# Kernel optimization log

Measured on AMD Instinct MI355X. Metric: run time of the kernel, lower is better.

## Reference

```python
import jax, jax.numpy as jnp
import numpy as np

N = 50000
D = 128
E = 600000
R = 8


def setup_inputs() -> dict:
    key = jax.random.key(0)
    ks = jax.random.split(key, 8)
    x = jax.random.normal(ks[0], (N, D), dtype=jnp.float32)
    edge_index = jax.random.randint(ks[1], (2, E), 0, N, dtype=jnp.int64)
    edge_type = jax.random.randint(ks[2], (E,), 0, R, dtype=jnp.int64)
    scale = 1.0 / np.sqrt(D)
    w1 = jax.random.normal(ks[3], (R, D, D), dtype=jnp.float32) * scale
    root1 = jax.random.normal(ks[4], (D, D), dtype=jnp.float32) * scale
    b1 = jnp.zeros((D,), dtype=jnp.float32)
    w2 = jax.random.normal(ks[5], (R, D, D), dtype=jnp.float32) * scale
    root2 = jax.random.normal(ks[6], (D, D), dtype=jnp.float32) * scale
    b2 = jnp.zeros((D,), dtype=jnp.float32)
    return {"x": x, "edge_index": edge_index, "edge_type": edge_type,
            "w1": w1, "root1": root1, "b1": b1,
            "w2": w2, "root2": root2, "b2": b2}


def _rgcn_conv(x, edge_index, edge_type, w, root, b):
    # PyG RGCNConv: per-relation MEAN aggregation of source features over
    # incoming edges, then relation-specific linear, summed over relations,
    # plus root transform and bias.
    src, dst = edge_index[0], edge_index[1]
    # combined segment id: (dst_node, relation) -> one segment_sum pass
    seg = dst * R + edge_type  # [E]
    msgs = x[src]              # [E, D] gather
    sums = jax.ops.segment_sum(msgs, seg, num_segments=N * R).reshape(N, R, D)
    cnts = jax.ops.segment_sum(jnp.ones((msgs.shape[0],), dtype=x.dtype), seg,
                               num_segments=N * R).reshape(N, R, 1)
    mean = sums / jnp.maximum(cnts, 1.0)  # [N, R, D]; empty -> 0
    out = jnp.einsum('nrd,rde->ne', mean, w) + x @ root + b
    return out


def reference(x, edge_index, edge_type, w1, root1, b1, w2, root2, b2):
    # dropout is identity in eval mode
    h = jax.nn.relu(_rgcn_conv(x, edge_index, edge_type, w1, root1, b1))
    out = jax.nn.relu(_rgcn_conv(h, edge_index, edge_type, w2, root2, b2))
    return out
```

## Files before the change

kernel.cpp:

```cpp
#include <hip/hip_runtime.h>

#define NN 50000
#define D 128
#define EE 600000
#define R 8
#define NR (NN * R)
#define SCAN_CHUNK 1024
#define NSB ((NR + SCAN_CHUNK - 1) / SCAN_CHUNK)
#define KO 1152

typedef unsigned short u16;
typedef unsigned int u32;
typedef __attribute__((ext_vector_type(8))) short bf16x8;
typedef __attribute__((ext_vector_type(4))) float f32x4;

__device__ inline u16 f2bf(float f) {
    union { float f; u32 u; } v; v.f = f;
    return (u16)((v.u + 0x7FFFu + ((v.u >> 16) & 1u)) >> 16);
}
__device__ inline float bf2f(u16 h) {
    union { u32 u; float f; } v; v.u = ((u32)h) << 16;
    return v.f;
}

__global__ __launch_bounds__(256) void xcast_kernel(const float2* __restrict__ x2,
                                                    u32* __restrict__ xb, int n) {
    int i = blockIdx.x * 256 + threadIdx.x;
    if (i < n) {
        float2 v = x2[i];
        xb[i] = (u32)f2bf(v.x) | ((u32)f2bf(v.y) << 16);
    }
}

__global__ __launch_bounds__(256) void hist_kernel(const int* __restrict__ dst,
                                                   const int* __restrict__ et,
                                                   int* __restrict__ cnt, int E) {
    int e = blockIdx.x * 256 + threadIdx.x;
    if (e < E) atomicAdd(&cnt[dst[e] * R + et[e]], 1);
}

__global__ __launch_bounds__(256) void scanA(const int* __restrict__ cnt,
                                             int* __restrict__ off,
                                             int* __restrict__ bsum) {
    __shared__ int ts[256];
    const int b = blockIdx.x, t = threadIdx.x;
    const int base = b * SCAN_CHUNK + t * 4;
    int v0 = 0, v1 = 0, v2 = 0, v3 = 0;
    if (base + 3 < NR) {
        int4 q = *(const int4*)(cnt + base);
        v0 = q.x; v1 = q.y; v2 = q.z; v3 = q.w;
    } else {
        if (base < NR) v0 = cnt[base];
        if (base + 1 < NR) v1 = cnt[base + 1];
        if (base + 2 < NR) v2 = cnt[base + 2];
    }
    const int s = v0 + v1 + v2 + v3;
    ts[t] = s;
    __syncthreads();
    for (int d = 1; d < 256; d <<= 1) {
        int x = (t >= d) ? ts[t - d] : 0;
        __syncthreads();
        ts[t] += x;
        __syncthreads();
    }
    const int excl = ts[t] - s;
    if (base < NR) off[base] = excl;
    if (base + 1 < NR) off[base + 1] = excl + v0;
    if (base + 2 < NR) off[base + 2] = excl + v0 + v1;
    if (base + 3 < NR) off[base + 3] = excl + v0 + v1 + v2;
    if (t == 255) bsum[b] = ts[255];
}

__global__ __launch_bounds__(512) void scanB(const int* __restrict__ bsum,
                                             int* __restrict__ boff) {
    __shared__ int ts[512];
    const int t = threadIdx.x;
    const int v = (t < NSB) ? bsum[t] : 0;
    ts[t] = v;
    __syncthreads();
    for (int d = 1; d < 512; d <<= 1) {
        int x = (t >= d) ? ts[t - d] : 0;
        __syncthreads();
        ts[t] += x;
        __syncthreads();
    }
    if (t < NSB) boff[t] = ts[t] - v;
}

__global__ __launch_bounds__(256) void scanC(int* __restrict__ off,
                                             int* __restrict__ cursor,
                                             const int* __restrict__ boff) {
    const int b = blockIdx.x, t = threadIdx.x;
    const int add = boff[b];
    const int base = b * SCAN_CHUNK + t * 4;
#pragma unroll
    for (int j = 0; j < 4; ++j)
        if (base + j < NR) {
            int v = off[base + j] + add;
            off[base + j] = v;
            cursor[base + j] = v;
        }
    if (b == 0 && t == 0) off[NR] = EE;
}

__global__ __launch_bounds__(256) void place_kernel(const int* __restrict__ src,
                                                    const int* __restrict__ dst,
                                                    const int* __restrict__ et,
                                                    const int* __restrict__ cnt,
                                                    int* __restrict__ cursor,
                                                    u32* __restrict__ epos,
                                                    float* __restrict__ scale, int E) {
    int e = blockIdx.x * 256 + threadIdx.x;
    if (e < E) {
        int r = et[e];
        int key = dst[e] * R + r;
        int p = atomicAdd(&cursor[key], 1);
        epos[p] = (u32)src[e] * (KO / 2) + (u32)r * (D / 2);
        scale[p] = 1.0f / (float)cnt[key];
    }
}

__global__ __launch_bounds__(256) void bprep2_kernel(const float* __restrict__ w1,
                                                     const float* __restrict__ root1,
                                                     u16* __restrict__ Bf1,
                                                     const float* __restrict__ w2,
                                                     const float* __restrict__ root2,
                                                     u16* __restrict__ Bf2) {
    int gidx = blockIdx.x * 256 + threadIdx.x;
    if (gidx >= 2 * 9 * 4 * 8 * 64) return;
    const int layer = gidx / (9 * 4 * 8 * 64);
    const int idx = gidx - layer * (9 * 4 * 8 * 64);
    const float* w = layer ? w2 : w1;
    const float* root = layer ? root2 : root1;
    u16* Bfrag = layer ? Bf2 : Bf1;
    const int lane = idx & 63;
    const int g = (idx >> 6) & 7;
    const int kc = (idx >> 9) & 3;
    const int ct = idx >> 11;
    const int col = ct * 128 + g * 16 + (lane & 15);
    const int kbase = kc * 32 + (lane >> 4) * 8;
    u16* o = Bfrag + (size_t)idx * 8;
#pragma unroll
    for (int j = 0; j < 8; ++j) {
        const int k = kbase + j;
        float v = (col < R * D) ? w[(size_t)(col >> 7) * (D * D) + (size_t)k * D + (col & 127)]
                                : root[(size_t)k * D + (col - R * D)];
        o[j] = f2bf(v);
    }
}

__global__ __launch_bounds__(256) void gemm_xw(const u16* __restrict__ xin,
                                               const u16* __restrict__ Bfrag,
                                               u16* __restrict__ y) {
    __shared__ uint4 Bs[2048];

    const int t = threadIdx.x;
    const int wave = t >> 6;
    const int lane = t & 63;
    const int quad = lane >> 4;
    const int l15 = lane & 15;
    const int n0 = blockIdx.x * 64;
    const int ct = blockIdx.y;
    const int n = n0 + wave * 16 + l15;
    const int nc = (n < NN) ? n : (NN - 1);

    const uint4* bsrc = (const uint4*)Bfrag + (size_t)ct * 2048;
    uint4 s[8];
#pragma unroll
    for (int i = 0; i < 8; ++i) s[i] = bsrc[t + 256 * i];

    const u16* xr = xin + (size_t)nc * D + quad * 8;
    bf16x8 a0 = *(const bf16x8*)(xr);
    bf16x8 a1 = *(const bf16x8*)(xr + 32);
    bf16x8 a2 = *(const bf16x8*)(xr + 64);
    bf16x8 a3 = *(const bf16x8*)(xr + 96);

#pragma unroll
    for (int i = 0; i < 8; ++i) Bs[t + 256 * i] = s[i];
    __syncthreads();

    f32x4 acc[8];
#pragma unroll
    for (int g = 0; g < 8; ++g) acc[g] = (f32x4){0.f, 0.f, 0.f, 0.f};

    const u16* bb = (const u16*)Bs + lane * 8;
#pragma unroll
    for (int g = 0; g < 8; ++g) {
        bf16x8 b0 = *(const bf16x8*)(bb + (0 * 8 + g) * 512);
        acc[g] = __builtin_amdgcn_mfma_f32_16x16x32_bf16(a0, b0, acc[g], 0, 0, 0);
        bf16x8 b1 = *(const bf16x8*)(bb + (1 * 8 + g) * 512);
        acc[g] = __builtin_amdgcn_mfma_f32_16x16x32_bf16(a1, b1, acc[g], 0, 0, 0);
        bf16x8 b2 = *(const bf16x8*)(bb + (2 * 8 + g) * 512);
        acc[g] = __builtin_amdgcn_mfma_f32_16x16x32_bf16(a2, b2, acc[g], 0, 0, 0);
        bf16x8 b3 = *(const bf16x8*)(bb + (3 * 8 + g) * 512);
        acc[g] = __builtin_amdgcn_mfma_f32_16x16x32_bf16(a3, b3, acc[g], 0, 0, 0);
    }

#pragma unroll
    for (int g = 0; g < 8; ++g) {
        const int col = ct * 128 + g * 16 + l15;
#pragma unroll
        for (int q = 0; q < 4; ++q) {
            const int row = n0 + wave * 16 + quad * 4 + q;
            if (row < NN)
                y[(size_t)row * KO + col] = f2bf(acc[g][q]);
        }
    }
}

template <bool OUTBF>
__global__ __launch_bounds__(256) void agg_kernel(const u32* __restrict__ yv,
                                                  const int* __restrict__ off,
                                                  const u32* __restrict__ epos,
                                                  const float* __restrict__ scale,
                                                  const float* __restrict__ bias,
                                                  void* __restrict__ outp) {
    const int n = blockIdx.x * 4 + (threadIdx.x >> 6);
    const int lane = threadIdx.x & 63;
    const int e0 = off[n * 8], e1 = off[n * 8 + 8];

    float ax = 0.f, ay = 0.f;
    int cbase = e0;
    u32 ed = 0; float sc = 0.f;
    if (cbase + lane < e1) { ed = epos[cbase + lane]; sc = scale[cbase + lane]; }

    int i = e0;
    while (i < e1) {
        const int chunk_end = (e1 < cbase + 64) ? e1 : (cbase + 64);
        for (; i + 1 < chunk_end; i += 2) {
            const int j0 = i - cbase;
            const u32 p0 = (u32)__shfl((int)ed, j0);
            const u32 p1 = (u32)__shfl((int)ed, j0 + 1);
            const float f0 = __shfl(sc, j0);
            const float f1 = __shfl(sc, j0 + 1);
            const u32 v0 = yv[(size_t)p0 + lane];
            const u32 v1 = yv[(size_t)p1 + lane];
            ax += f0 * bf2f((u16)(v0 & 0xFFFFu));
            ay += f0 * bf2f((u16)(v0 >> 16));
            ax += f1 * bf2f((u16)(v1 & 0xFFFFu));
            ay += f1 * bf2f((u16)(v1 >> 16));
        }
        if (i < chunk_end) {
            const int j0 = i - cbase;
            const u32 p0 = (u32)__shfl((int)ed, j0);
            const float f0 = __shfl(sc, j0);
            const u32 v0 = yv[(size_t)p0 + lane];
            ax += f0 * bf2f((u16)(v0 & 0xFFFFu));
            ay += f0 * bf2f((u16)(v0 >> 16));
            ++i;
        }
        if (i < e1) {
            cbase += 64;
            const bool ok = (cbase + lane < e1);
            ed = ok ? epos[cbase + lane] : 0;
            sc = ok ? scale[cbase + lane] : 0.f;
        }
    }

    const u32 rv = yv[(size_t)n * (KO / 2) + (R * D / 2) + lane];
    const float2 bb = ((const float2*)bias)[lane];
    const float ox = fmaxf(ax + bf2f((u16)(rv & 0xFFFFu)) + bb.x, 0.f);
    const float oy = fmaxf(ay + bf2f((u16)(rv >> 16)) + bb.y, 0.f);
    if (OUTBF)
        ((u32*)outp)[(size_t)n * 64 + lane] = (u32)f2bf(ox) | ((u32)f2bf(oy) << 16);
    else
        ((float2*)outp)[(size_t)n * 64 + lane] = make_float2(ox, oy);
}

extern "C" void kernel_launch(void* const* d_in, const int* in_sizes, int n_in,
                              void* d_out, int out_size, void* d_ws, size_t ws_size,
                              hipStream_t stream) {
    const float* x = (const float*)d_in[0];
    const int* ei = (const int*)d_in[1];
    const int* et = (const int*)d_in[2];
    const float* w1 = (const float*)d_in[3];
    const float* root1 = (const float*)d_in[4];
    const float* b1 = (const float*)d_in[5];
    const float* w2 = (const float*)d_in[6];
    const float* root2 = (const float*)d_in[7];
    const float* b2 = (const float*)d_in[8];
    float* out = (float*)d_out;

    char* ws = (char*)d_ws;
    int* off    = (int*)(ws + 0);
    int* cnt_i  = (int*)(ws + 1600512);
    int* cursor = (int*)(ws + 3200512);
    int* bsum   = (int*)(ws + 4800512);
    int* boff   = (int*)(ws + 4802304);
    u32* epos   = (u32*)(ws + 4804096);
    float* scl  = (float*)(ws + 7204096);
    u32* xb     = (u32*)(ws + 9604096);
    u32* h      = (u32*)(ws + 22404096);
    u16* y      = (u16*)(ws + 35204096);
    u16* Bf1    = (u16*)(ws + 150404096);
    u16* Bf2    = (u16*)(ws + 150699008);

    const int* srcp = ei;
    const int* dstp = ei + EE;

    xcast_kernel<<<(NN * D / 2 + 255) / 256, 256, 0, stream>>>((const float2*)x,
                                                               xb, NN * D / 2);
    hipMemsetAsync(cnt_i, 0, (size_t)NR * sizeof(int), stream);
    hist_kernel<<<(EE + 255) / 256, 256, 0, stream>>>(dstp, et, cnt_i, EE);
    scanA<<<NSB, 256, 0, stream>>>(cnt_i, off, bsum);
    scanB<<<1, 512, 0, stream>>>(bsum, boff);
    scanC<<<NSB, 256, 0, stream>>>(off, cursor, boff);
    place_kernel<<<(EE + 255) / 256, 256, 0, stream>>>(srcp, dstp, et, cnt_i,
                                                       cursor, epos, scl, EE);
    bprep2_kernel<<<(2 * 9 * 4 * 8 * 64 + 255) / 256, 256, 0, stream>>>(
        w1, root1, Bf1, w2, root2, Bf2);

    const dim3 ggrid((NN + 63) / 64, 9);
    const int agg_blocks = NN / 4;

    gemm_xw<<<ggrid, 256, 0, stream>>>((const u16*)xb, Bf1, y);
    agg_kernel<true><<<agg_blocks, 256, 0, stream>>>((const u32*)y, off, epos,
                                                     scl, b1, h);

    gemm_xw<<<ggrid, 256, 0, stream>>>((const u16*)h, Bf2, y);
    agg_kernel<false><<<agg_blocks, 256, 0, stream>>>((const u32*)y, off, epos,
                                                      scl, b2, out);
}
```

Baseline: 310.0 us.

## Loop GEMM over column tiles per block, pack edge data, unroll gather by four

The GEMM now launches one block per 64-row tile and loops over all 9 column tiles inside the block. The A fragments are loaded once and reused, and each B tile is restaged through shared memory with extra barriers, but the grid is 9x smaller and tiles are processed serially. Edge source offset and mean scale are packed into one uint2 array so the aggregation does a single load per edge. The gather loop is unrolled to four edges per iteration to raise memory-level parallelism.

```diff
diff --git a/kernel.cpp b/kernel.cpp
--- a/kernel.cpp
+++ b/kernel.cpp
@@ -108,15 +108,15 @@
                                                     const int* __restrict__ et,
                                                     const int* __restrict__ cnt,
                                                     int* __restrict__ cursor,
-                                                    u32* __restrict__ epos,
-                                                    float* __restrict__ scale, int E) {
+                                                    uint2* __restrict__ edat, int E) {
     int e = blockIdx.x * 256 + threadIdx.x;
     if (e < E) {
         int r = et[e];
         int key = dst[e] * R + r;
         int p = atomicAdd(&cursor[key], 1);
-        epos[p] = (u32)src[e] * (KO / 2) + (u32)r * (D / 2);
-        scale[p] = 1.0f / (float)cnt[key];
+        float s = 1.0f / (float)cnt[key];
+        edat[p] = make_uint2((u32)src[e] * (KO / 2) + (u32)r * (D / 2),
+                             __float_as_uint(s));
     }
 }
 
@@ -160,14 +160,8 @@
     const int quad = lane >> 4;
     const int l15 = lane & 15;
     const int n0 = blockIdx.x * 64;
-    const int ct = blockIdx.y;
     const int n = n0 + wave * 16 + l15;
     const int nc = (n < NN) ? n : (NN - 1);
-
-    const uint4* bsrc = (const uint4*)Bfrag + (size_t)ct * 2048;
-    uint4 s[8];
-#pragma unroll
-    for (int i = 0; i < 8; ++i) s[i] = bsrc[t + 256 * i];
 
     const u16* xr = xin + (size_t)nc * D + quad * 8;
     bf16x8 a0 = *(const bf16x8*)(xr);
@@ -175,35 +169,44 @@
     bf16x8 a2 = *(const bf16x8*)(xr + 64);
     bf16x8 a3 = *(const bf16x8*)(xr + 96);
 
-#pragma unroll
-    for (int i = 0; i < 8; ++i) Bs[t + 256 * i] = s[i];
-    __syncthreads();
-
-    f32x4 acc[8];
-#pragma unroll
-    for (int g = 0; g < 8; ++g) acc[g] = (f32x4){0.f, 0.f, 0.f, 0.f};
-
-    const u16* bb = (const u16*)Bs + lane * 8;
-#pragma unroll
-    for (int g = 0; g < 8; ++g) {
-        bf16x8 b0 = *(const bf16x8*)(bb + (0 * 8 + g) * 512);
-        acc[g] = __builtin_amdgcn_mfma_f32_16x16x32_bf16(a0, b0, acc[g], 0, 0, 0);
-        bf16x8 b1 = *(const bf16x8*)(bb + (1 * 8 + g) * 512);
-        acc[g] = __builtin_amdgcn_mfma_f32_16x16x32_bf16(a1, b1, acc[g], 0, 0, 0);
-        bf16x8 b2 = *(const bf16x8*)(bb + (2 * 8 + g) * 512);
-        acc[g] = __builtin_amdgcn_mfma_f32_16x16x32_bf16(a2, b2, acc[g], 0, 0, 0);
-        bf16x8 b3 = *(const bf16x8*)(bb + (3 * 8 + g) * 512);
-        acc[g] = __builtin_amdgcn_mfma_f32_16x16x32_bf16(a3, b3, acc[g], 0, 0, 0);
-    }
-
-#pragma unroll
-    for (int g = 0; g < 8; ++g) {
-        const int col = ct * 128 + g * 16 + l15;
-#pragma unroll
-        for (int q = 0; q < 4; ++q) {
-            const int row = n0 + wave * 16 + quad * 4 + q;
-            if (row < NN)
-                y[(size_t)row * KO + col] = f2bf(acc[g][q]);
+#pragma unroll 1
+    for (int ct = 0; ct < 9; ++ct) {
+        const uint4* bsrc = (const uint4*)Bfrag + (size_t)ct * 2048;
+        uint4 s[8];
+#pragma unroll
+        for (int i = 0; i < 8; ++i) s[i] = bsrc[t + 256 * i];
+
+        __syncthreads();
+#pragma unroll
+        for (int i = 0; i < 8; ++i) Bs[t + 256 * i] = s[i];
+        __syncthreads();
+
+        f32x4 acc[8];
+#pragma unroll
+        for (int g = 0; g < 8; ++g) acc[g] = (f32x4){0.f, 0.f, 0.f, 0.f};
+
+        const u16* bb = (const u16*)Bs + lane * 8;
+#pragma unroll
+        for (int g = 0; g < 8; ++g) {
+            bf16x8 b0 = *(const bf16x8*)(bb + (0 * 8 + g) * 512);
+            acc[g] = __builtin_amdgcn_mfma_f32_16x16x32_bf16(a0, b0, acc[g], 0, 0, 0);
+            bf16x8 b1 = *(const bf16x8*)(bb + (1 * 8 + g) * 512);
+            acc[g] = __builtin_amdgcn_mfma_f32_16x16x32_bf16(a1, b1, acc[g], 0, 0, 0);
+            bf16x8 b2 = *(const bf16x8*)(bb + (2 * 8 + g) * 512);
+            acc[g] = __builtin_amdgcn_mfma_f32_16x16x32_bf16(a2, b2, acc[g], 0, 0, 0);
+            bf16x8 b3 = *(const bf16x8*)(bb + (3 * 8 + g) * 512);
+            acc[g] = __builtin_amdgcn_mfma_f32_16x16x32_bf16(a3, b3, acc[g], 0, 0, 0);
+        }
+
+#pragma unroll
+        for (int g = 0; g < 8; ++g) {
+            const int col = ct * 128 + g * 16 + l15;
+#pragma unroll
+            for (int q = 0; q < 4; ++q) {
+                const int row = n0 + wave * 16 + quad * 4 + q;
+                if (row < NN)
+                    y[(size_t)row * KO + col] = f2bf(acc[g][q]);
+            }
         }
     }
 }
@@ -211,8 +214,7 @@
 template <bool OUTBF>
 __global__ __launch_bounds__(256) void agg_kernel(const u32* __restrict__ yv,
                                                   const int* __restrict__ off,
-                                                  const u32* __restrict__ epos,
-                                                  const float* __restrict__ scale,
+                                                  const uint2* __restrict__ edat,
                                                   const float* __restrict__ bias,
                                                   void* __restrict__ outp) {
     const int n = blockIdx.x * 4 + (threadIdx.x >> 6);
@@ -221,39 +223,42 @@
 
     float ax = 0.f, ay = 0.f;
     int cbase = e0;
-    u32 ed = 0; float sc = 0.f;
-    if (cbase + lane < e1) { ed = epos[cbase + lane]; sc = scale[cbase + lane]; }
+    uint2 ev = make_uint2(0u, 0u);
+    if (cbase + lane < e1) ev = edat[cbase + lane];
 
     int i = e0;
     while (i < e1) {
         const int chunk_end = (e1 < cbase + 64) ? e1 : (cbase + 64);
-        for (; i + 1 < chunk_end; i += 2) {
-            const int j0 = i - cbase;
-            const u32 p0 = (u32)__shfl((int)ed, j0);
-            const u32 p1 = (u32)__shfl((int)ed, j0 + 1);
-            const float f0 = __shfl(sc, j0);
-            const float f1 = __shfl(sc, j0 + 1);
+        for (; i + 3 < chunk_end; i += 4) {
+            const int j = i - cbase;
+            const u32 p0 = (u32)__shfl((int)ev.x, j);
+            const u32 p1 = (u32)__shfl((int)ev.x, j + 1);
+            const u32 p2 = (u32)__shfl((int)ev.x, j + 2);
+            const u32 p3 = (u32)__shfl((int)ev.x, j + 3);
+            const float f0 = __uint_as_float((u32)__shfl((int)ev.y, j));
+            const float f1 = __uint_as_float((u32)__shfl((int)ev.y, j + 1));
+            const float f2 = __uint_as_float((u32)__shfl((int)ev.y, j + 2));
+            const float f3 = __uint_as_float((u32)__shfl((int)ev.y, j + 3));
             const u32 v0 = yv[(size_t)p0 + lane];
             const u32 v1 = yv[(size_t)p1 + lane];
-            ax += f0 * bf2f((u16)(v0 & 0xFFFFu));
-            ay += f0 * bf2f((u16)(v0 >> 16));
-            ax += f1 * bf2f((u16)(v1 & 0xFFFFu));
-            ay += f1 * bf2f((u16)(v1 >> 16));
-        }
-        if (i < chunk_end) {
-            const int j0 = i - cbase;
-            const u32 p0 = (u32)__shfl((int)ed, j0);
-            const float f0 = __shfl(sc, j0);
+            const u32 v2 = yv[(size_t)p2 + lane];
+            const u32 v3 = yv[(size_t)p3 + lane];
+            ax += f0 * bf2f((u16)(v0 & 0xFFFFu)); ay += f0 * bf2f((u16)(v0 >> 16));
+            ax += f1 * bf2f((u16)(v1 & 0xFFFFu)); ay += f1 * bf2f((u16)(v1 >> 16));
+            ax += f2 * bf2f((u16)(v2 & 0xFFFFu)); ay += f2 * bf2f((u16)(v2 >> 16));
+            ax += f3 * bf2f((u16)(v3 & 0xFFFFu)); ay += f3 * bf2f((u16)(v3 >> 16));
+        }
+        for (; i < chunk_end; ++i) {
+            const int j = i - cbase;
+            const u32 p0 = (u32)__shfl((int)ev.x, j);
+            const float f0 = __uint_as_float((u32)__shfl((int)ev.y, j));
             const u32 v0 = yv[(size_t)p0 + lane];
             ax += f0 * bf2f((u16)(v0 & 0xFFFFu));
             ay += f0 * bf2f((u16)(v0 >> 16));
-            ++i;
         }
         if (i < e1) {
             cbase += 64;
-            const bool ok = (cbase + lane < e1);
-            ed = ok ? epos[cbase + lane] : 0;
-            sc = ok ? scale[cbase + lane] : 0.f;
+            ev = (cbase + lane < e1) ? edat[cbase + lane] : make_uint2(0u, 0u);
         }
     }
 
@@ -287,8 +292,7 @@
     int* cursor = (int*)(ws + 3200512);
     int* bsum   = (int*)(ws + 4800512);
     int* boff   = (int*)(ws + 4802304);
-    u32* epos   = (u32*)(ws + 4804096);
-    float* scl  = (float*)(ws + 7204096);
+    uint2* edat = (uint2*)(ws + 4804096);
     u32* xb     = (u32*)(ws + 9604096);
     u32* h      = (u32*)(ws + 22404096);
     u16* y      = (u16*)(ws + 35204096);
@@ -306,18 +310,18 @@
     scanB<<<1, 512, 0, stream>>>(bsum, boff);
     scanC<<<NSB, 256, 0, stream>>>(off, cursor, boff);
     place_kernel<<<(EE + 255) / 256, 256, 0, stream>>>(srcp, dstp, et, cnt_i,
-                                                       cursor, epos, scl, EE);
+                                                       cursor, edat, EE);
     bprep2_kernel<<<(2 * 9 * 4 * 8 * 64 + 255) / 256, 256, 0, stream>>>(
         w1, root1, Bf1, w2, root2, Bf2);
 
-    const dim3 ggrid((NN + 63) / 64, 9);
+    const int gemm_blocks = (NN + 63) / 64;
     const int agg_blocks = NN / 4;
 
-    gemm_xw<<<ggrid, 256, 0, stream>>>((const u16*)xb, Bf1, y);
-    agg_kernel<true><<<agg_blocks, 256, 0, stream>>>((const u32*)y, off, epos,
-                                                     scl, b1, h);
-
-    gemm_xw<<<ggrid, 256, 0, stream>>>((const u16*)h, Bf2, y);
-    agg_kernel<false><<<agg_blocks, 256, 0, stream>>>((const u32*)y, off, epos,
-                                                      scl, b2, out);
-}
+    gemm_xw<<<gemm_blocks, 256, 0, stream>>>((const u16*)xb, Bf1, y);
+    agg_kernel<true><<<agg_blocks, 256, 0, stream>>>((const u32*)y, off, edat,
+                                                     b1, h);
+
+    gemm_xw<<<gemm_blocks, 256, 0, stream>>>((const u16*)h, Bf2, y);
+    agg_kernel<false><<<agg_blocks, 256, 0, stream>>>((const u32*)y, off, edat,
+                                                      b2, out);
+}
```

Result: slower. 434.4 us (+40.1%).
